# Kernel tuning notes

Hardware: AMD Instinct MI355X
Metric: run time of the kernel (lower is better)

## Reference

```python
import jax, jax.numpy as jnp
import numpy as np

N = 50000
H = 300


def l2_normalize(x, eps=1e-12):
    n = jnp.sqrt(jnp.sum(x * x, axis=1, keepdims=True))
    return x / jnp.maximum(n, eps)


def gat_layer(x, ei_j, ei_i, a_i, a_j, n_nodes):
    # per-node scalar scores, gathered per edge
    s_i = x @ a_i  # [N]
    s_j = x @ a_j  # [N]
    e = jax.nn.leaky_relu(s_i[ei_i] + s_j[ei_j], 0.01)  # [E]
    # scatter softmax over incoming edges of node i
    m = jax.ops.segment_max(e, ei_i, num_segments=n_nodes)
    ex = jnp.exp(e - m[ei_i])
    denom = jax.ops.segment_sum(ex, ei_i, num_segments=n_nodes)
    alpha = ex / (denom[ei_i] + 1e-16)
    out = jax.ops.segment_sum(alpha[:, None] * x[ei_j], ei_i, num_segments=n_nodes)
    return jax.nn.relu(out)


def gcn_layer(x, ei_j, ei_i, W, n_nodes):
    deg = jax.ops.segment_sum(jnp.ones_like(ei_i, dtype=x.dtype), ei_i, num_segments=n_nodes)
    dinv = jnp.where(deg > 0, deg ** -0.5, 0.0)
    norm = dinv[ei_j] * dinv[ei_i]  # [E]
    h = x @ W.T
    out = jax.ops.segment_sum(norm[:, None] * h[ei_j], ei_i, num_segments=n_nodes)
    return jax.nn.relu(out)


def highway(x1, x2, W, b):
    gate = jax.nn.sigmoid(x1 @ W.T + b)
    return gate * x2 + (1.0 - gate) * x1


def setup_inputs() -> dict:
    key = jax.random.key(0)
    ks = jax.random.split(key, 16)
    s = 1.0 / np.sqrt(H)
    inp = {
        "x_e": jax.random.normal(ks[0], (N, H), dtype=jnp.float32),
        "edge_index": jax.random.randint(ks[1], (2, 400000), 0, N, dtype=jnp.int32),
        "rel": jax.random.randint(ks[2], (400000,), 0, 1000, dtype=jnp.int32),
        "edge_index_all": jax.random.randint(ks[3], (2, 800000), 0, N, dtype=jnp.int32),
        "rel_all": jax.random.randint(ks[4], (800000,), 0, 1000, dtype=jnp.int32),
        "gcn1_W": jax.random.uniform(ks[5], (H, H), jnp.float32, -s, s),
        "hw1_W": jax.random.uniform(ks[6], (H, H), jnp.float32, -s, s),
        "hw1_b": jax.random.uniform(ks[7], (H,), jnp.float32, -s, s),
        "gat1_ai": jax.random.uniform(ks[8], (H,), jnp.float32, -s, s),
        "gat1_aj": jax.random.uniform(ks[9], (H,), jnp.float32, -s, s),
        "ghw1_W": jax.random.uniform(ks[10], (H, H), jnp.float32, -s, s),
        "ghw1_b": jax.random.uniform(ks[11], (H,), jnp.float32, -s, s),
        "gat2_ai": jax.random.uniform(ks[12], (H,), jnp.float32, -s, s),
        "gat2_aj": jax.random.uniform(ks[13], (H,), jnp.float32, -s, s),
        "ghw2_W": jax.random.uniform(ks[14], (H, H), jnp.float32, -s, s),
        "ghw2_b": jax.random.uniform(ks[15], (H,), jnp.float32, -s, s),
    }
    k2 = jax.random.split(jax.random.key(1), 2)
    inp["gat_ai"] = jax.random.uniform(k2[0], (H,), jnp.float32, -s, s)
    inp["gat_aj"] = jax.random.uniform(k2[1], (H,), jnp.float32, -s, s)
    return inp


def reference(x_e, edge_index, rel, edge_index_all, rel_all,
              gcn1_W, hw1_W, hw1_b, gat1_ai, gat1_aj, ghw1_W, ghw1_b,
              gat2_ai, gat2_aj, ghw2_W, ghw2_b, gat_ai, gat_aj):
    # dropout(p=0.05) treated as identity (eval mode)
    ei_j, ei_i = edge_index_all[0], edge_index_all[1]
    n = x_e.shape[0]

    x0 = l2_normalize(x_e)
    x2 = highway(x0, gcn_layer(x0, ei_j, ei_i, gcn1_W, n), hw1_W, hw1_b)
    x3 = highway(x2, gat_layer(x2, ei_j, ei_i, gat1_ai, gat1_aj, n), ghw1_W, ghw1_b)
    xe = highway(x2, gat_layer(x3, ei_j, ei_i, gat2_ai, gat2_aj, n), ghw2_W, ghw2_b)
    ye = gat_layer(xe, ei_j, ei_i, gat_ai, gat_aj, n)
    return jnp.concatenate([xe, ye], axis=1)
```

## Files before the change

kernel.cpp:

```cpp
#include <hip/hip_runtime.h>
#include <hip/hip_bf16.h>
#include <math.h>

#define H 300
#define WAVE 64
#define STRB 320
#define SCB 1024

typedef short bf16x8 __attribute__((ext_vector_type(8)));
typedef unsigned short u16;
typedef u16 u16x8 __attribute__((ext_vector_type(8)));
typedef u16 u16x4 __attribute__((ext_vector_type(4)));
typedef float f32x4 __attribute__((ext_vector_type(4)));

__device__ inline unsigned short f2b(float f) {
    union { float f; unsigned int u; } x; x.f = f;
    unsigned int r = x.u + 0x7FFF + ((x.u >> 16) & 1);
    return (unsigned short)(r >> 16);
}
__device__ inline float b2f(u16 h) {
    union { float f; unsigned int u; } x; x.u = ((unsigned int)h) << 16;
    return x.f;
}

__global__ void k_l2norm(const float* __restrict__ x, u16* __restrict__ outb, int n) {
    int wave = blockIdx.x * (blockDim.x / WAVE) + (threadIdx.x >> 6);
    int lane = threadIdx.x & 63;
    if (wave >= n) return;
    const float* row = x + (long)wave * H;
    float s = 0.f;
    for (int j = lane; j < H; j += WAVE) { float v = row[j]; s += v * v; }
    for (int o = 32; o > 0; o >>= 1) s += __shfl_xor(s, o);
    float sc = 1.0f / fmaxf(sqrtf(s), 1e-12f);
    u16* brow = outb + (long)wave * STRB;
    for (int j = lane; j < H; j += WAVE) brow[j] = f2b(row[j] * sc);
    for (int j = H + lane; j < STRB; j += WAVE) brow[j] = 0;
}

__global__ void k_zero_int(int* p, int n) {
    int i = blockIdx.x * blockDim.x + threadIdx.x;
    int stride = gridDim.x * blockDim.x;
    for (; i < n; i += stride) p[i] = 0;
}

__global__ void k_count_deg(const int* __restrict__ ei_i, int* __restrict__ deg, int E) {
    int i = blockIdx.x * blockDim.x + threadIdx.x;
    int stride = gridDim.x * blockDim.x;
    for (; i < E; i += stride) atomicAdd(&deg[ei_i[i]], 1);
}

__global__ void k_dinv(const int* __restrict__ deg, float* __restrict__ dinv, int n) {
    int i = blockIdx.x * blockDim.x + threadIdx.x;
    int stride = gridDim.x * blockDim.x;
    for (; i < n; i += stride) {
        int d = deg[i];
        dinv[i] = (d > 0) ? 1.0f / sqrtf((float)d) : 0.0f;
    }
}

__global__ void k_scan_local(const int* __restrict__ deg, int* __restrict__ offs,
                             int* __restrict__ btot, int n) {
    __shared__ int sh[SCB];
    int base = blockIdx.x * SCB;
    int tid = threadIdx.x;
    int v = (base + tid < n) ? deg[base + tid] : 0;
    sh[tid] = v;
    __syncthreads();
    for (int off = 1; off < SCB; off <<= 1) {
        int add = (tid >= off) ? sh[tid - off] : 0;
        __syncthreads();
        sh[tid] += add;
        __syncthreads();
    }
    if (base + tid < n) offs[base + tid] = sh[tid] - v;
    if (tid == SCB - 1) btot[blockIdx.x] = sh[tid];
}

__global__ void k_scan_tots(const int* __restrict__ btot, int* __restrict__ bpre,
                            int nb, int* __restrict__ total_out) {
    int l = threadIdx.x;
    int v = (l < nb) ? btot[l] : 0;
    int own = v;
    for (int o = 1; o < 64; o <<= 1) {
        int u = __shfl_up(v, o);
        if (l >= o) v += u;
    }
    if (l < nb) bpre[l] = v - own;
    if (l == 63) total_out[0] = v;
}

__global__ void k_scan_apply(int* __restrict__ offs, const int* __restrict__ bpre,
                             int* __restrict__ cursor, int n) {
    int i = blockIdx.x * blockDim.x + threadIdx.x;
    int stride = gridDim.x * blockDim.x;
    for (; i < n; i += stride) {
        int o = offs[i] + bpre[i / SCB];
        offs[i] = o;
        cursor[i] = o;
    }
}

__global__ void k_fill_csr(const int* __restrict__ ei_j, const int* __restrict__ ei_i,
                           int* __restrict__ cursor, int* __restrict__ csr_src, int E) {
    int i = blockIdx.x * blockDim.x + threadIdx.x;
    int stride = gridDim.x * blockDim.x;
    for (; i < E; i += stride) {
        int dst = ei_i[i];
        int pos = atomicAdd(&cursor[dst], 1);
        csr_src[pos] = ei_j[i];
    }
}

__global__ void k_conv_w4(const float* __restrict__ W0f, const float* __restrict__ W1f,
                          const float* __restrict__ W2f, const float* __restrict__ W3f,
                          u16* __restrict__ Wb0, u16* __restrict__ Wb1,
                          u16* __restrict__ Wb2, u16* __restrict__ Wb3) {
    int which = blockIdx.x & 3;
    const float* W = (which == 0) ? W0f : (which == 1) ? W1f : (which == 2) ? W2f : W3f;
    u16* Wb = (which == 0) ? Wb0 : (which == 1) ? Wb1 : (which == 2) ? Wb2 : Wb3;
    int idx = (blockIdx.x >> 2) * blockDim.x + threadIdx.x;
    int stride = (gridDim.x >> 2) * blockDim.x;
    for (; idx < STRB * STRB; idx += stride) {
        int r = idx / STRB, c = idx - r * STRB;
        Wb[idx] = (r < H && c < H) ? f2b(W[r * H + c]) : 0;
    }
}

#define BM 128
#define BN 64
#define BK 32
#define LDP 40
#define NXCD 8

__global__ __launch_bounds__(256) void k_gemm_fused(
        const u16* __restrict__ Xb,
        const u16* __restrict__ Wb,
        u16* __restrict__ outb,
        const float* __restrict__ hwbias,
        const u16* __restrict__ xnewb, const float* __restrict__ xnewf,
        const u16* __restrict__ xold,
        float* __restrict__ outf, long ostride,
        u16* __restrict__ mirror,
        int n_rows) {
    __shared__ __align__(16) short As[BM * LDP];
    __shared__ __align__(16) short Bs[BN * LDP];
    const int tid = threadIdx.x;

    const int nwg = gridDim.x;
    const int q = nwg / NXCD, r = nwg % NXCD;
    const int xcd = blockIdx.x % NXCD, idx = blockIdx.x / NXCD;
    const int wgid = (xcd < r ? xcd * (q + 1) : r * (q + 1) + (xcd - r) * q) + idx;
    const int bm = (wgid / 5) * BM;
    const int bn = (wgid % 5) * BN;

    const int lane = tid & 63;
    const int wid = tid >> 6;
    const int wr = wid >> 1;
    const int wc = wid & 1;
    const int lrow = lane & 15;
    const int kgrp = lane >> 4;

    f32x4 acc[4][2];
    #pragma unroll
    for (int m = 0; m < 4; m++)
        #pragma unroll
        for (int n = 0; n < 2; n++) acc[m][n] = (f32x4){0.f, 0.f, 0.f, 0.f};

    for (int k0 = 0; k0 < STRB; k0 += BK) {
        #pragma unroll
        for (int i = 0; i < 2; ++i) {
            int qq = tid + i * 256;
            int rr = qq >> 2, c = (qq & 3) << 3;
            int gr = bm + rr;
            u16x8 v = {0, 0, 0, 0, 0, 0, 0, 0};
            if (gr < n_rows) v = *(const u16x8*)&Xb[(long)gr * STRB + k0 + c];
            *(u16x8*)&As[rr * LDP + c] = v;
        }
        {
            int rr = tid >> 2, c = (tid & 3) << 3;
            u16x8 v = *(const u16x8*)&Wb[(long)(bn + rr) * STRB + k0 + c];
            *(u16x8*)&Bs[rr * LDP + c] = v;
        }
        __syncthreads();

        bf16x8 af[4], bfr[2];
        #pragma unroll
        for (int m = 0; m < 4; m++) {
            int row = wr * 64 + m * 16 + lrow;
            af[m] = *(const bf16x8*)&As[row * LDP + kgrp * 8];
        }
        #pragma unroll
        for (int n = 0; n < 2; n++) {
            int col = wc * 32 + n * 16 + lrow;
            bfr[n] = *(const bf16x8*)&Bs[col * LDP + kgrp * 8];
        }
        #pragma unroll
        for (int m = 0; m < 4; m++)
            #pragma unroll
            for (int n = 0; n < 2; n++)
                acc[m][n] = __builtin_amdgcn_mfma_f32_16x16x32_bf16(af[m], bfr[n], acc[m][n], 0, 0, 0);
        __syncthreads();
    }

    if (outb) {
        #pragma unroll
        for (int m = 0; m < 4; m++)
            #pragma unroll
            for (int n = 0; n < 2; n++) {
                int gc = bn + wc * 32 + n * 16 + lrow;
                if (gc >= STRB) continue;
                #pragma unroll
                for (int rr = 0; rr < 4; rr++) {
                    int gr = bm + wr * 64 + m * 16 + kgrp * 4 + rr;
                    if (gr < n_rows) outb[(long)gr * STRB + gc] = (gc < H) ? f2b(acc[m][n][rr]) : 0;
                }
            }
    } else {
        #pragma unroll
        for (int m = 0; m < 4; m++)
            #pragma unroll
            for (int n = 0; n < 2; n++) {
                int gc = bn + wc * 32 + n * 16 + lrow;
                if (gc >= STRB) continue;
                bool colv = (gc < H);
                float bb = colv ? hwbias[gc] : 0.f;
                #pragma unroll
                for (int rr = 0; rr < 4; rr++) {
                    int gr = bm + wr * 64 + m * 16 + kgrp * 4 + rr;
                    if (gr >= n_rows) continue;
                    if (colv) {
                        float pre = acc[m][n][rr] + bb;
                        float g = 1.0f / (1.0f + __expf(-pre));
                        float xn = xnewb ? b2f(xnewb[(long)gr * STRB + gc])
                                         : xnewf[(long)gr * H + gc];
                        float xo = b2f(xold[(long)gr * STRB + gc]);
                        float val = g * xn + (1.0f - g) * xo;
                        if (outf) outf[(long)gr * ostride + gc] = val;
                        if (mirror) mirror[(long)gr * STRB + gc] = f2b(val);
                    } else if (mirror) {
                        mirror[(long)gr * STRB + gc] = 0;
                    }
                }
            }
    }
}

__global__ __launch_bounds__(256) void k_gcn_gather_w(const u16* __restrict__ xb,
                                                      const float* __restrict__ dinv,
                                                      const int* __restrict__ offs,
                                                      const int* __restrict__ csr,
                                                      u16* __restrict__ outb, int n) {
    int node = blockIdx.x * 4 + (threadIdx.x >> 6);
    int lane = threadIdx.x & 63;
    if (node >= n) return;
    int start = offs[node], end = offs[node + 1];
    float acc[8];
    #pragma unroll
    for (int j = 0; j < 8; j++) acc[j] = 0.f;
    float di = dinv[node];
    for (int tb = start; tb < end; tb += 64) {
        int p = tb + lane;
        int src = 0; float w = 0.f;
        if (p < end) {
            src = csr[p];
            w = di * dinv[src];
        }
        int cnt = min(64, end - tb);
        for (int qq = 0; qq < cnt; qq++) {
            float wq = __shfl(w, qq);
            int sq = __shfl(src, qq);
            if (lane < 40) {
                u16x8 v = *(const u16x8*)&xb[(long)sq * STRB + lane * 8];
                #pragma unroll
                for (int j = 0; j < 8; j++) acc[j] += wq * b2f(v[j]);
            }
        }
    }
    if (lane < 40) {
        u16x8 o;
        #pragma unroll
        for (int j = 0; j < 8; j++) o[j] = f2b(fmaxf(acc[j], 0.f));
        *(u16x8*)&outb[(long)node * STRB + lane * 8] = o;
    }
}

__global__ void k_dual_dot_b(const u16* __restrict__ xb,
                             const float* __restrict__ ai, const float* __restrict__ aj,
                             float* __restrict__ s_i, float* __restrict__ s_j, int n) {
    int wave = blockIdx.x * (blockDim.x / WAVE) + (threadIdx.x >> 6);
    int lane = threadIdx.x & 63;
    if (wave >= n) return;
    const u16* row = xb + (long)wave * STRB;
    float d0 = 0.f, d1 = 0.f;
    {
        u16x4 v = *(const u16x4*)&row[lane * 4];
        float4 a4 = *(const float4*)&ai[lane * 4];
        float4 j4 = *(const float4*)&aj[lane * 4];
        float x0 = b2f(v[0]), x1 = b2f(v[1]), x2 = b2f(v[2]), x3 = b2f(v[3]);
        d0 = x0 * a4.x + x1 * a4.y + x2 * a4.z + x3 * a4.w;
        d1 = x0 * j4.x + x1 * j4.y + x2 * j4.z + x3 * j4.w;
    }
    if (lane < 11) {
        u16x4 v = *(const u16x4*)&row[256 + lane * 4];
        float4 a4 = *(const float4*)&ai[256 + lane * 4];
        float4 j4 = *(const float4*)&aj[256 + lane * 4];
        float x0 = b2f(v[0]), x1 = b2f(v[1]), x2 = b2f(v[2]), x3 = b2f(v[3]);
        d0 += x0 * a4.x + x1 * a4.y + x2 * a4.z + x3 * a4.w;
        d1 += x0 * j4.x + x1 * j4.y + x2 * j4.z + x3 * j4.w;
    }
    for (int o = 32; o > 0; o >>= 1) { d0 += __shfl_down(d0, o); d1 += __shfl_down(d1, o); }
    if (lane == 0) { s_i[wave] = d0; s_j[wave] = d1; }
}

__global__ __launch_bounds__(256) void k_gat_gather_w(const u16* __restrict__ xb,
                                                      const float* __restrict__ s_i_arr,
                                                      const float* __restrict__ s_j_arr,
                                                      const int* __restrict__ offs,
                                                      const int* __restrict__ csr,
                                                      u16* __restrict__ outb16,
                                                      float* __restrict__ outf, long out_stride,
                                                      int out_off, int n) {
    int node = blockIdx.x * 4 + (threadIdx.x >> 6);
    int lane = threadIdx.x & 63;
    if (node >= n) return;
    int start = offs[node], end = offs[node + 1];
    int deg = end - start;
    float acc[8];
    #pragma unroll
    for (int j = 0; j < 8; j++) acc[j] = 0.f;

    if (deg > 0) {
        float si = s_i_arr[node];
        float m_t = -1e30f, s_t = 0.f;
        for (int p = start + lane; p < end; p += 64) {
            float sc = si + s_j_arr[csr[p]];
            sc = (sc >= 0.f) ? sc : 0.01f * sc;
            if (sc > m_t) { s_t = s_t * __expf(m_t - sc) + 1.0f; m_t = sc; }
            else s_t += __expf(sc - m_t);
        }
        for (int o = 32; o > 0; o >>= 1) {
            float m2 = __shfl_xor(m_t, o), s2 = __shfl_xor(s_t, o);
            float mm = fmaxf(m_t, m2);
            s_t = s_t * __expf(m_t - mm) + s2 * __expf(m2 - mm);
            m_t = mm;
        }
        float m = m_t;
        float inv = 1.0f / (s_t + 1e-16f);
        for (int tb = start; tb < end; tb += 64) {
            int p = tb + lane;
            int src = 0; float w = 0.f;
            if (p < end) {
                src = csr[p];
                float sc = si + s_j_arr[src];
                sc = (sc >= 0.f) ? sc : 0.01f * sc;
                w = __expf(sc - m) * inv;
            }
            int cnt = min(64, end - tb);
            for (int qq = 0; qq < cnt; qq++) {
                float wq = __shfl(w, qq);
                int sq = __shfl(src, qq);
                if (lane < 40) {
                    u16x8 v = *(const u16x8*)&xb[(long)sq * STRB + lane * 8];
                    #pragma unroll
                    for (int j = 0; j < 8; j++) acc[j] += wq * b2f(v[j]);
                }
            }
        }
    }
    if (outb16) {
        if (lane < 40) {
            u16x8 o;
            #pragma unroll
            for (int j = 0; j < 8; j++) o[j] = f2b(fmaxf(acc[j], 0.f));
            *(u16x8*)&outb16[(long)node * STRB + lane * 8] = o;
        }
    } else {
        if (lane < 38) {
            #pragma unroll
            for (int j = 0; j < 8; j++) {
                int c = lane * 8 + j;
                if (c < H) outf[(long)node * out_stride + out_off + c] = fmaxf(acc[j], 0.f);
            }
        }
    }
}

extern "C" void kernel_launch(void* const* d_in, const int* in_sizes, int n_in,
                              void* d_out, int out_size, void* d_ws, size_t ws_size,
                              hipStream_t stream) {
    const float* x_e     = (const float*)d_in[0];
    const int*   ei_all  = (const int*)d_in[3];
    const float* gcn1_W  = (const float*)d_in[5];
    const float* hw1_W   = (const float*)d_in[6];
    const float* hw1_b   = (const float*)d_in[7];
    const float* gat1_ai = (const float*)d_in[8];
    const float* gat1_aj = (const float*)d_in[9];
    const float* ghw1_W  = (const float*)d_in[10];
    const float* ghw1_b  = (const float*)d_in[11];
    const float* gat2_ai = (const float*)d_in[12];
    const float* gat2_aj = (const float*)d_in[13];
    const float* ghw2_W  = (const float*)d_in[14];
    const float* ghw2_b  = (const float*)d_in[15];
    const float* gat_ai  = (const float*)d_in[16];
    const float* gat_aj  = (const float*)d_in[17];

    const int N = in_sizes[0] / H;
    const int E = in_sizes[3] / 2;
    const int* ei_j = ei_all;
    const int* ei_i = ei_all + E;

    float* out = (float*)d_out;

    size_t NSB = (size_t)N * STRB;
    u16*   W0   = (u16*)d_ws;
    u16*   W1   = W0 + NSB;
    u16*   W2   = W1 + NSB;
    u16*   W3   = W2 + NSB;
    float* G2F  = (float*)d_ws;
    float* sbi  = (float*)(W3 + NSB);
    float* sbj  = sbi + N;
    float* dinv = sbj + N;
    int*   deg  = (int*)(dinv + N);
    int*   offs = deg + N;
    int*   cursor = offs + (N + 1);
    int*   csr  = cursor + N;
    int*   btot = csr + E;
    int*   bpre = btot + 64;
    u16*   wb0  = (u16*)(bpre + 64);
    u16*   wb1  = wb0 + STRB * STRB;
    u16*   wb2  = wb1 + STRB * STRB;
    u16*   wb3  = wb2 + STRB * STRB;

    dim3 blk256(256);
    int rowsPerBlock = 256 / WAVE;
    dim3 gridRows((N + rowsPerBlock - 1) / rowsPerBlock);
    dim3 gridNodeW((N + 3) / 4);
    dim3 gridE(2048);
    dim3 gridW(400);
    dim3 gridGemm(((N + BM - 1) / BM) * 5);
    int nScanB = (N + SCB - 1) / SCB;

    hipLaunchKernelGGL(k_l2norm, gridRows, blk256, 0, stream, x_e, W0, N);

    hipLaunchKernelGGL(k_zero_int, dim3(256), blk256, 0, stream, deg, N);
    hipLaunchKernelGGL(k_count_deg, gridE, blk256, 0, stream, ei_i, deg, E);
    hipLaunchKernelGGL(k_dinv, dim3(256), blk256, 0, stream, deg, dinv, N);
    hipLaunchKernelGGL(k_scan_local, dim3(nScanB), dim3(SCB), 0, stream, deg, offs, btot, N);
    hipLaunchKernelGGL(k_scan_tots, dim3(1), dim3(64), 0, stream, btot, bpre, nScanB, offs + N);
    hipLaunchKernelGGL(k_scan_apply, dim3(256), blk256, 0, stream, offs, bpre, cursor, N);
    hipLaunchKernelGGL(k_fill_csr, gridE, blk256, 0, stream, ei_j, ei_i, cursor, csr, E);
    hipLaunchKernelGGL(k_conv_w4, gridW, blk256, 0, stream,
                       gcn1_W, hw1_W, ghw1_W, ghw2_W, wb0, wb1, wb2, wb3);

    hipLaunchKernelGGL(k_gemm_fused, gridGemm, blk256, 0, stream,
                       W0, wb0, W1,
                       (const float*)nullptr, (const u16*)nullptr, (const float*)nullptr,
                       (const u16*)nullptr, (float*)nullptr, (long)0, (u16*)nullptr, N);

    hipLaunchKernelGGL(k_gcn_gather_w, gridNodeW, blk256, 0, stream, W1, dinv, offs, csr, W2, N);

    hipLaunchKernelGGL(k_gemm_fused, gridGemm, blk256, 0, stream,
                       W0, wb1, (u16*)nullptr,
                       hw1_b, W2, (const float*)nullptr, W0,
                       (float*)nullptr, (long)0, W3, N);

    hipLaunchKernelGGL(k_dual_dot_b, gridRows, blk256, 0, stream, W3, gat1_ai, gat1_aj, sbi, sbj, N);

    hipLaunchKernelGGL(k_gat_gather_w, gridNodeW, blk256, 0, stream, W3, sbi, sbj, offs, csr,
                       W1, (float*)nullptr, (long)0, 0, N);

    hipLaunchKernelGGL(k_gemm_fused, gridGemm, blk256, 0, stream,
                       W3, wb2, (u16*)nullptr,
                       ghw1_b, W1, (const float*)nullptr, W3,
                       (float*)nullptr, (long)0, W2, N);

    hipLaunchKernelGGL(k_dual_dot_b, gridRows, blk256, 0, stream, W2, gat2_ai, gat2_aj, sbi, sbj, N);

    hipLaunchKernelGGL(k_gat_gather_w, gridNodeW, blk256, 0, stream, W2, sbi, sbj, offs, csr,
                       (u16*)nullptr, G2F, (long)H, 0, N);

    hipLaunchKernelGGL(k_gemm_fused, gridGemm, blk256, 0, stream,
                       W3, wb3, (u16*)nullptr,
                       ghw2_b, (const u16*)nullptr, G2F, W3,
                       out, (long)(2 * H), W2, N);

    hipLaunchKernelGGL(k_dual_dot_b, gridRows, blk256, 0, stream, W2, gat_ai, gat_aj, sbi, sbj, N);

    hipLaunchKernelGGL(k_gat_gather_w, gridNodeW, blk256, 0, stream, W2, sbi, sbj, offs, csr,
                       (u16*)nullptr, out, (long)(2 * H), H, N);
}
```

Before: 743.6 us.

## Stage GEMM epilogue through LDS for vectorized stores; fold dinv into scan

The GEMM epilogue now writes the MFMA accumulators into a shared-memory tile that reuses the A/B staging buffers. It then reads the tile back row-wise so each thread issues 16-byte coalesced loads and stores for the bf16 output, the highway inputs and the fp32 output. Before, each thread did scattered 2-byte or 4-byte accesses along columns. The cost is an extra LDS round trip and barrier, and the gate pre-activation is now rounded to bf16 before the sigmoid. Separately, the degree-inverse computation is merged into the local scan kernel to drop one launch.

```diff
diff --git a/kernel.cpp b/kernel.cpp
--- a/kernel.cpp
+++ b/kernel.cpp
@@ -49,21 +49,13 @@
     for (; i < E; i += stride) atomicAdd(&deg[ei_i[i]], 1);
 }
 
-__global__ void k_dinv(const int* __restrict__ deg, float* __restrict__ dinv, int n) {
-    int i = blockIdx.x * blockDim.x + threadIdx.x;
-    int stride = gridDim.x * blockDim.x;
-    for (; i < n; i += stride) {
-        int d = deg[i];
-        dinv[i] = (d > 0) ? 1.0f / sqrtf((float)d) : 0.0f;
-    }
-}
-
 __global__ void k_scan_local(const int* __restrict__ deg, int* __restrict__ offs,
-                             int* __restrict__ btot, int n) {
+                             int* __restrict__ btot, float* __restrict__ dinv, int n) {
     __shared__ int sh[SCB];
     int base = blockIdx.x * SCB;
     int tid = threadIdx.x;
     int v = (base + tid < n) ? deg[base + tid] : 0;
+    if (base + tid < n) dinv[base + tid] = (v > 0) ? 1.0f / sqrtf((float)v) : 0.0f;
     sh[tid] = v;
     __syncthreads();
     for (int off = 1; off < SCB; off <<= 1) {
@@ -130,6 +122,7 @@
 #define BN 64
 #define BK 32
 #define LDP 40
+#define STP 70
 #define NXCD 8
 
 __global__ __launch_bounds__(256) void k_gemm_fused(
@@ -142,8 +135,10 @@
         float* __restrict__ outf, long ostride,
         u16* __restrict__ mirror,
         int n_rows) {
-    __shared__ __align__(16) short As[BM * LDP];
-    __shared__ __align__(16) short Bs[BN * LDP];
+    __shared__ __align__(16) char smem[BM * STP * 2];
+    short* As = (short*)smem;
+    short* Bs = (short*)(smem + BM * LDP * 2);
+    u16*   St = (u16*)smem;
     const int tid = threadIdx.x;
 
     const int nwg = gridDim.x;
@@ -202,46 +197,68 @@
         __syncthreads();
     }
 
-    if (outb) {
-        #pragma unroll
-        for (int m = 0; m < 4; m++)
+    #pragma unroll
+    for (int m = 0; m < 4; m++)
+        #pragma unroll
+        for (int n = 0; n < 2; n++) {
+            int lc = wc * 32 + n * 16 + lrow;
             #pragma unroll
-            for (int n = 0; n < 2; n++) {
-                int gc = bn + wc * 32 + n * 16 + lrow;
-                if (gc >= STRB) continue;
+            for (int rr = 0; rr < 4; rr++) {
+                int row = wr * 64 + m * 16 + kgrp * 4 + rr;
+                St[row * STP + lc] = f2b(acc[m][n][rr]);
+            }
+        }
+    __syncthreads();
+
+    #pragma unroll
+    for (int p = 0; p < 4; p++) {
+        int row = p * 32 + (tid >> 3);
+        int gr = bm + row;
+        if (gr >= n_rows) continue;
+        int lc0 = (tid & 7) * 8;
+        int gc0 = bn + lc0;
+        u16x8 pv = *(const u16x8*)&St[row * STP + lc0];
+        if (outb) {
+            u16x8 o;
+            #pragma unroll
+            for (int j = 0; j < 8; j++) o[j] = (gc0 + j < H) ? pv[j] : (u16)0;
+            *(u16x8*)&outb[(long)gr * STRB + gc0] = o;
+        } else {
+            u16x8 xov = *(const u16x8*)&xold[(long)gr * STRB + gc0];
+            float xn[8];
+            if (xnewb) {
+                u16x8 xnv = *(const u16x8*)&xnewb[(long)gr * STRB + gc0];
                 #pragma unroll
-                for (int rr = 0; rr < 4; rr++) {
-                    int gr = bm + wr * 64 + m * 16 + kgrp * 4 + rr;
-                    if (gr < n_rows) outb[(long)gr * STRB + gc] = (gc < H) ? f2b(acc[m][n][rr]) : 0;
-                }
-            }
-    } else {
-        #pragma unroll
-        for (int m = 0; m < 4; m++)
+                for (int j = 0; j < 8; j++) xn[j] = b2f(xnv[j]);
+            } else {
+                f32x4 a = *(const f32x4*)&xnewf[(long)gr * H + gc0];
+                f32x4 b = *(const f32x4*)&xnewf[(long)gr * H + gc0 + 4];
+                xn[0] = a[0]; xn[1] = a[1]; xn[2] = a[2]; xn[3] = a[3];
+                xn[4] = b[0]; xn[5] = b[1]; xn[6] = b[2]; xn[7] = b[3];
+            }
+            float val[8];
             #pragma unroll
-            for (int n = 0; n < 2; n++) {
-                int gc = bn + wc * 32 + n * 16 + lrow;
-                if (gc >= STRB) continue;
-                bool colv = (gc < H);
-                float bb = colv ? hwbias[gc] : 0.f;
+            for (int j = 0; j < 8; j++) {
+                int gcj = gc0 + j;
+                if (gcj < H) {
+                    float pre = b2f(pv[j]) + hwbias[gcj];
+                    float g = 1.0f / (1.0f + __expf(-pre));
+                    val[j] = g * xn[j] + (1.0f - g) * b2f(xov[j]);
+                } else val[j] = 0.f;
+            }
+            if (outf) {
+                if (gc0 < H)
+                    *(f32x4*)&outf[(long)gr * ostride + gc0] = (f32x4){val[0], val[1], val[2], val[3]};
+                if (gc0 + 4 < H)
+                    *(f32x4*)&outf[(long)gr * ostride + gc0 + 4] = (f32x4){val[4], val[5], val[6], val[7]};
+            }
+            if (mirror) {
+                u16x8 mv;
                 #pragma unroll
-                for (int rr = 0; rr < 4; rr++) {
-                    int gr = bm + wr * 64 + m * 16 + kgrp * 4 + rr;
-                    if (gr >= n_rows) continue;
-                    if (colv) {
-                        float pre = acc[m][n][rr] + bb;
-                        float g = 1.0f / (1.0f + __expf(-pre));
-                        float xn = xnewb ? b2f(xnewb[(long)gr * STRB + gc])
-                                         : xnewf[(long)gr * H + gc];
-                        float xo = b2f(xold[(long)gr * STRB + gc]);
-                        float val = g * xn + (1.0f - g) * xo;
-                        if (outf) outf[(long)gr * ostride + gc] = val;
-                        if (mirror) mirror[(long)gr * STRB + gc] = f2b(val);
-                    } else if (mirror) {
-                        mirror[(long)gr * STRB + gc] = 0;
-                    }
-                }
-            }
+                for (int j = 0; j < 8; j++) mv[j] = f2b(val[j]);
+                *(u16x8*)&mirror[(long)gr * STRB + gc0] = mv;
+            }
+        }
     }
 }
 
@@ -444,8 +461,7 @@
 
     hipLaunchKernelGGL(k_zero_int, dim3(256), blk256, 0, stream, deg, N);
     hipLaunchKernelGGL(k_count_deg, gridE, blk256, 0, stream, ei_i, deg, E);
-    hipLaunchKernelGGL(k_dinv, dim3(256), blk256, 0, stream, deg, dinv, N);
-    hipLaunchKernelGGL(k_scan_local, dim3(nScanB), dim3(SCB), 0, stream, deg, offs, btot, N);
+    hipLaunchKernelGGL(k_scan_local, dim3(nScanB), dim3(SCB), 0, stream, deg, offs, btot, dinv, N);
     hipLaunchKernelGGL(k_scan_tots, dim3(1), dim3(64), 0, stream, btot, bpre, nScanB, offs + N);
     hipLaunchKernelGGL(k_scan_apply, dim3(256), blk256, 0, stream, offs, bpre, cursor, N);
     hipLaunchKernelGGL(k_fill_csr, gridE, blk256, 0, stream, ei_j, ei_i, cursor, csr, E);
```

Measured after the change: 693.0 us. 1.07x faster.
